# Optimization experiments

Measured on AMD Instinct MI355X. Metric: run time of the kernel, lower is better.

## Reference

```python
import jax, jax.numpy as jnp
import numpy as np

EPS = 1e-6


def setup_inputs() -> dict:
    key = jax.random.key(0)
    kx, ky = jax.random.split(key)
    B, C, H, W = 8, 128, 48, 64
    x = jax.random.normal(kx, (B, C, H, W), dtype=jnp.float32)
    y = jax.random.normal(ky, (B, C, H, W), dtype=jnp.float32)
    return {"x": x, "y": y}


def reference(x, y):
    # x, y: (b, c, h, w)
    b, c, h, w = x.shape
    # torch: x.transpose(2,3).view(b,c,h*w) -> x flattened w-major,
    #        so output channel k = v*h + u corresponds to x[:, :, u, v].
    # corr5[b, v, u, i, j] = sum_c x[b,c,u,v] * y[b,c,i,j]
    corr = jnp.einsum('bcuv,bcij->bvuij', x, y)
    corr = corr.reshape(b, w * h, h, w)  # channel k = v*h + u
    # normalization: ReLU then L2-normalize over the h*w channel dim
    corr = jax.nn.relu(corr)
    norm = jnp.sqrt(jnp.sum(corr * corr, axis=1, keepdims=True) + EPS)
    return corr / norm
```

## Files before the change

kernel.cpp:

```cpp
#include <hip/hip_runtime.h>
#include <hip/hip_bf16.h>

#define NB 8
#define NC 128
#define NH 48
#define NW 64
#define NS 3072
#define EPSF 1e-6f

#define GLOBAL_AS __attribute__((address_space(1)))
#define LDS_AS __attribute__((address_space(3)))

typedef __bf16 bf16x8 __attribute__((ext_vector_type(8)));
typedef float f32x4 __attribute__((ext_vector_type(4)));

__global__ __launch_bounds__(256) void transpose_both(
    const float* __restrict__ x, const float* __restrict__ y,
    __hip_bfloat16* __restrict__ AT, __hip_bfloat16* __restrict__ BT) {
  __shared__ float tile[32][65];
  const int id = blockIdx.x;
  const int b = id & 7;
  const int which = (id >> 3) & 1;
  const int rr = id >> 4;
  const int f0 = (rr % 96) * 32, c0 = (rr / 96) * 64;
  const float* src = which ? y : x;
  __hip_bfloat16* dst = which ? BT : AT;
  const int t = threadIdx.x;

  const int fi = t & 31, ci0 = t >> 5;
  const float* sp = src + ((size_t)b * NC + c0) * NS + f0;
#pragma unroll
  for (int i = 0; i < 8; ++i) {
    int ci = ci0 + i * 8;
    tile[fi][ci] = sp[(size_t)ci * NS + fi];
  }
  __syncthreads();

  const int co = t & 63, fo0 = t >> 6;
#pragma unroll
  for (int i = 0; i < 8; ++i) {
    int fo = fo0 + i * 4;
    int f = f0 + fo;
    int k = which ? f : ((f & 63) * NH + (f >> 6));
    dst[((size_t)b * NS + k) * NC + c0 + co] = __float2bfloat16(tile[fo][co]);
  }
}

template <bool WRITE>
__global__ __launch_bounds__(256, 2) void corr_gemm(
    const __hip_bfloat16* __restrict__ AT,
    const __hip_bfloat16* __restrict__ BT,
    const float* __restrict__ part_in, float* __restrict__ part_out,
    float* __restrict__ out) {
  __shared__ char smem[66560];
  float* rnc = (float*)(smem + 65536);
  const int id = blockIdx.x;
  const int b = id & 7;
  const int tl = id >> 3;
  const int mt = tl / 24, nt = tl - mt * 24;
  const int t = threadIdx.x;
  const int lane = t & 63, wid = t >> 6;
  const int wm = wid >> 1, wn = wid & 1;
  const int l15 = lane & 15, kg = lane >> 4;

  const char* Ag = (const char*)(AT + ((size_t)b * NS + mt * 128) * NC);
  const char* Bg = (const char*)(BT + ((size_t)b * NS + nt * 128) * NC);
  {
    const int lr = lane >> 4, lg = lane & 15;
#pragma unroll
    for (int i = 0; i < 8; ++i) {
      int c = wid * 8 + i;
      int row = c * 4 + lr;
      int g = lg ^ (row & 7);
      int go = row * 256 + g * 16;
      __builtin_amdgcn_global_load_lds((const GLOBAL_AS unsigned*)(Ag + go),
                                       (LDS_AS unsigned*)(smem + c * 1024),
                                       16, 0, 0);
      __builtin_amdgcn_global_load_lds(
          (const GLOBAL_AS unsigned*)(Bg + go),
          (LDS_AS unsigned*)(smem + 32768 + c * 1024), 16, 0, 0);
    }
  }
  if (WRITE) {
    if (t < 128) {
      float s = 0.f;
#pragma unroll
      for (int q = 0; q < 24; ++q)
        s += part_in[(size_t)q * (NB * NS) + (size_t)b * NS + nt * 128 + t];
      rnc[t] = rsqrtf(s + EPSF);
    }
  }
  __syncthreads();

  f32x4 acc[4][4] = {};
  const int rx = l15 & 7;
#pragma unroll
  for (int kk = 0; kk < 4; ++kk) {
    int g = (kk * 4 + kg) ^ rx;
    bf16x8 a[4], bb[4];
#pragma unroll
    for (int mi = 0; mi < 4; ++mi) {
      int row = wm * 64 + mi * 16 + l15;
      a[mi] = *(const bf16x8*)(smem + row * 256 + g * 16);
    }
#pragma unroll
    for (int ni = 0; ni < 4; ++ni) {
      int row = wn * 64 + ni * 16 + l15;
      bb[ni] = *(const bf16x8*)(smem + 32768 + row * 256 + g * 16);
    }
#pragma unroll
    for (int mi = 0; mi < 4; ++mi)
#pragma unroll
      for (int ni = 0; ni < 4; ++ni)
        acc[mi][ni] = __builtin_amdgcn_mfma_f32_16x16x32_bf16(
            a[mi], bb[ni], acc[mi][ni], 0, 0, 0);
  }

  if (!WRITE) {
    float cs[4] = {0.f, 0.f, 0.f, 0.f};
#pragma unroll
    for (int ni = 0; ni < 4; ++ni)
#pragma unroll
      for (int mi = 0; mi < 4; ++mi)
#pragma unroll
        for (int r = 0; r < 4; ++r) {
          float v = fmaxf(acc[mi][ni][r], 0.f);
          cs[ni] += v * v;
        }
#pragma unroll
    for (int ni = 0; ni < 4; ++ni) {
      cs[ni] += __shfl_xor(cs[ni], 16, 64);
      cs[ni] += __shfl_xor(cs[ni], 32, 64);
    }
    __syncthreads();
    float* csum = (float*)smem;
    if (kg == 0) {
#pragma unroll
      for (int ni = 0; ni < 4; ++ni)
        csum[wm * 128 + wn * 64 + ni * 16 + l15] = cs[ni];
    }
    __syncthreads();
    if (t < 128) {
      float s = csum[t] + csum[128 + t];
      part_out[(size_t)mt * (NB * NS) + (size_t)b * NS + nt * 128 + t] = s;
    }
  } else {
    float rnv[4];
#pragma unroll
    for (int ni = 0; ni < 4; ++ni) rnv[ni] = rnc[wn * 64 + ni * 16 + l15];
    __syncthreads();

    float* tf = (float*)smem;
#pragma unroll
    for (int mi = 0; mi < 4; ++mi)
#pragma unroll
      for (int ni = 0; ni < 4; ++ni)
#pragma unroll
        for (int r = 0; r < 4; ++r) {
          int row = wm * 64 + mi * 16 + kg * 4 + r;
          int col = wn * 64 + ni * 16 + l15;
          tf[row * 129 + col] = fmaxf(acc[mi][ni][r], 0.f) * rnv[ni];
        }
    __syncthreads();

    float* ob = out + (size_t)b * NS * NS + (size_t)(mt * 128) * NS + nt * 128;
    const int rsub = t >> 5, c4 = (t & 31) * 4;
#pragma unroll
    for (int it = 0; it < 16; ++it) {
      int row = it * 8 + rsub;
      f32x4 v = *(const f32x4*)&tf[row * 129 + c4];
      *(f32x4*)&ob[(size_t)row * NS + c4] = v;
    }
  }
}

extern "C" void kernel_launch(void* const* d_in, const int* in_sizes, int n_in,
                              void* d_out, int out_size, void* d_ws,
                              size_t ws_size, hipStream_t stream) {
  const float* x = (const float*)d_in[0];
  const float* y = (const float*)d_in[1];
  float* out = (float*)d_out;
  char* ws = (char*)d_ws;

  const size_t AT_OFF = 0;
  const size_t BT_OFF = 6291456;
  const size_t PART_OFF = 12582912;
  const size_t NEED = 14942208;
  if (ws_size < NEED) return;

  __hip_bfloat16* AT = (__hip_bfloat16*)(ws + AT_OFF);
  __hip_bfloat16* BT = (__hip_bfloat16*)(ws + BT_OFF);
  float* part = (float*)(ws + PART_OFF);

  dim3 tb(256);
  transpose_both<<<dim3(3072), tb, 0, stream>>>(x, y, AT, BT);
  corr_gemm<false><<<dim3(4608), tb, 0, stream>>>(AT, BT, nullptr, part,
                                                  nullptr);
  corr_gemm<true><<<dim3(4608), tb, 0, stream>>>(AT, BT, part, nullptr, out);
}
```

Measured before the change: 112.6 us.

## Split output GEMM into wider 128x256 tile kernel with chunked epilogue and nontemporal stores

Separates the partial-norm pass and the output pass into distinct kernels. The output pass now uses 512-thread blocks covering a 128x256 tile, which halves the block count and reuses each A tile across twice the columns. The epilogue stages the tile through LDS in two 64-row chunks and writes it with nontemporal stores. This targets the write-bound output phase, reducing per-block overhead and cache pollution from the roughly 300MB output, at the cost of higher LDS use per block and extra barriers.

```diff
diff --git a/kernel.cpp b/kernel.cpp
--- a/kernel.cpp
+++ b/kernel.cpp
@@ -46,14 +46,10 @@
   }
 }
 
-template <bool WRITE>
-__global__ __launch_bounds__(256, 2) void corr_gemm(
+__global__ __launch_bounds__(256, 2) void corr_part(
     const __hip_bfloat16* __restrict__ AT,
-    const __hip_bfloat16* __restrict__ BT,
-    const float* __restrict__ part_in, float* __restrict__ part_out,
-    float* __restrict__ out) {
-  __shared__ char smem[66560];
-  float* rnc = (float*)(smem + 65536);
+    const __hip_bfloat16* __restrict__ BT, float* __restrict__ part_out) {
+  __shared__ char smem[65536];
   const int id = blockIdx.x;
   const int b = id & 7;
   const int tl = id >> 3;
@@ -81,15 +77,6 @@
           (LDS_AS unsigned*)(smem + 32768 + c * 1024), 16, 0, 0);
     }
   }
-  if (WRITE) {
-    if (t < 128) {
-      float s = 0.f;
-#pragma unroll
-      for (int q = 0; q < 24; ++q)
-        s += part_in[(size_t)q * (NB * NS) + (size_t)b * NS + nt * 128 + t];
-      rnc[t] = rsqrtf(s + EPSF);
-    }
-  }
   __syncthreads();
 
   f32x4 acc[4][4] = {};
@@ -99,15 +86,12 @@
     int g = (kk * 4 + kg) ^ rx;
     bf16x8 a[4], bb[4];
 #pragma unroll
-    for (int mi = 0; mi < 4; ++mi) {
-      int row = wm * 64 + mi * 16 + l15;
-      a[mi] = *(const bf16x8*)(smem + row * 256 + g * 16);
-    }
-#pragma unroll
-    for (int ni = 0; ni < 4; ++ni) {
-      int row = wn * 64 + ni * 16 + l15;
-      bb[ni] = *(const bf16x8*)(smem + 32768 + row * 256 + g * 16);
-    }
+    for (int mi = 0; mi < 4; ++mi)
+      a[mi] = *(const bf16x8*)(smem + (wm * 64 + mi * 16 + l15) * 256 + g * 16);
+#pragma unroll
+    for (int ni = 0; ni < 4; ++ni)
+      bb[ni] = *(const bf16x8*)(smem + 32768 +
+                                (wn * 64 + ni * 16 + l15) * 256 + g * 16);
 #pragma unroll
     for (int mi = 0; mi < 4; ++mi)
 #pragma unroll
@@ -116,61 +100,133 @@
             a[mi], bb[ni], acc[mi][ni], 0, 0, 0);
   }
 
-  if (!WRITE) {
-    float cs[4] = {0.f, 0.f, 0.f, 0.f};
+  float cs[4] = {0.f, 0.f, 0.f, 0.f};
+#pragma unroll
+  for (int ni = 0; ni < 4; ++ni)
+#pragma unroll
+    for (int mi = 0; mi < 4; ++mi)
+#pragma unroll
+      for (int r = 0; r < 4; ++r) {
+        float v = fmaxf(acc[mi][ni][r], 0.f);
+        cs[ni] += v * v;
+      }
+#pragma unroll
+  for (int ni = 0; ni < 4; ++ni) {
+    cs[ni] += __shfl_xor(cs[ni], 16, 64);
+    cs[ni] += __shfl_xor(cs[ni], 32, 64);
+  }
+  __syncthreads();
+  float* csum = (float*)smem;
+  if (kg == 0) {
 #pragma unroll
     for (int ni = 0; ni < 4; ++ni)
+      csum[wm * 128 + wn * 64 + ni * 16 + l15] = cs[ni];
+  }
+  __syncthreads();
+  if (t < 128) {
+    float s = csum[t] + csum[128 + t];
+    part_out[(size_t)mt * (NB * NS) + (size_t)b * NS + nt * 128 + t] = s;
+  }
+}
+
+__global__ __launch_bounds__(512, 2) void corr_out256(
+    const __hip_bfloat16* __restrict__ AT,
+    const __hip_bfloat16* __restrict__ BT, const float* __restrict__ part_in,
+    float* __restrict__ out) {
+  __shared__ char smem[99328];
+  float* rnc = (float*)(smem + 98304);
+  const int id = blockIdx.x;
+  const int b = id & 7;
+  const int tl = id >> 3;
+  const int mt = tl / 12, nt = tl - mt * 12;
+  const int t = threadIdx.x;
+  const int lane = t & 63, wid = t >> 6;
+  const int wm = wid >> 2, wn = wid & 3;
+  const int l15 = lane & 15, kg = lane >> 4;
+
+  const char* Ag = (const char*)(AT + ((size_t)b * NS + mt * 128) * NC);
+  const char* Bg = (const char*)(BT + ((size_t)b * NS + nt * 256) * NC);
+  {
+    const int lr = lane >> 4, lg = lane & 15;
+#pragma unroll
+    for (int i = 0; i < 4; ++i) {
+      int c = wid * 4 + i;
+      int row = c * 4 + lr;
+      int g = lg ^ (row & 7);
+      __builtin_amdgcn_global_load_lds(
+          (const GLOBAL_AS unsigned*)(Ag + row * 256 + g * 16),
+          (LDS_AS unsigned*)(smem + c * 1024), 16, 0, 0);
+    }
+#pragma unroll
+    for (int i = 0; i < 8; ++i) {
+      int c = wid * 8 + i;
+      int row = c * 4 + lr;
+      int g = lg ^ (row & 7);
+      __builtin_amdgcn_global_load_lds(
+          (const GLOBAL_AS unsigned*)(Bg + row * 256 + g * 16),
+          (LDS_AS unsigned*)(smem + 32768 + c * 1024), 16, 0, 0);
+    }
+  }
+  if (t < 256) {
+    float s = 0.f;
+#pragma unroll
+    for (int q = 0; q < 24; ++q)
+      s += part_in[(size_t)q * (NB * NS) + (size_t)b * NS + nt * 256 + t];
+    rnc[t] = rsqrtf(s + EPSF);
+  }
+  __syncthreads();
+
+  f32x4 acc[4][4] = {};
+  const int rx = l15 & 7;
+#pragma unroll
+  for (int kk = 0; kk < 4; ++kk) {
+    int g = (kk * 4 + kg) ^ rx;
+    bf16x8 a[4], bb[4];
+#pragma unroll
+    for (int mi = 0; mi < 4; ++mi)
+      a[mi] = *(const bf16x8*)(smem + (wm * 64 + mi * 16 + l15) * 256 + g * 16);
+#pragma unroll
+    for (int ni = 0; ni < 4; ++ni)
+      bb[ni] = *(const bf16x8*)(smem + 32768 +
+                                (wn * 64 + ni * 16 + l15) * 256 + g * 16);
+#pragma unroll
+    for (int mi = 0; mi < 4; ++mi)
+#pragma unroll
+      for (int ni = 0; ni < 4; ++ni)
+        acc[mi][ni] = __builtin_amdgcn_mfma_f32_16x16x32_bf16(
+            a[mi], bb[ni], acc[mi][ni], 0, 0, 0);
+  }
+
+  float rnv[4];
+#pragma unroll
+  for (int ni = 0; ni < 4; ++ni) rnv[ni] = rnc[wn * 64 + ni * 16 + l15];
+  __syncthreads();
+
+  float* tf = (float*)smem;
+  float* ob = out + (size_t)b * NS * NS + (size_t)(mt * 128) * NS + nt * 256;
+#pragma unroll
+  for (int ch = 0; ch < 2; ++ch) {
+    if (wm == ch) {
 #pragma unroll
       for (int mi = 0; mi < 4; ++mi)
 #pragma unroll
-        for (int r = 0; r < 4; ++r) {
-          float v = fmaxf(acc[mi][ni][r], 0.f);
-          cs[ni] += v * v;
-        }
-#pragma unroll
-    for (int ni = 0; ni < 4; ++ni) {
-      cs[ni] += __shfl_xor(cs[ni], 16, 64);
-      cs[ni] += __shfl_xor(cs[ni], 32, 64);
+        for (int ni = 0; ni < 4; ++ni)
+#pragma unroll
+          for (int r = 0; r < 4; ++r) {
+            int row = mi * 16 + kg * 4 + r;
+            int col = wn * 64 + ni * 16 + l15;
+            tf[row * 258 + col] = fmaxf(acc[mi][ni][r], 0.f) * rnv[ni];
+          }
     }
     __syncthreads();
-    float* csum = (float*)smem;
-    if (kg == 0) {
-#pragma unroll
-      for (int ni = 0; ni < 4; ++ni)
-        csum[wm * 128 + wn * 64 + ni * 16 + l15] = cs[ni];
+#pragma unroll
+    for (int it = 0; it < 8; ++it) {
+      int rl = wid + it * 8;
+      f32x4 v = *(const f32x4*)&tf[rl * 258 + lane * 4];
+      __builtin_nontemporal_store(
+          v, (f32x4*)&ob[(size_t)(ch * 64 + rl) * NS + lane * 4]);
     }
     __syncthreads();
-    if (t < 128) {
-      float s = csum[t] + csum[128 + t];
-      part_out[(size_t)mt * (NB * NS) + (size_t)b * NS + nt * 128 + t] = s;
-    }
-  } else {
-    float rnv[4];
-#pragma unroll
-    for (int ni = 0; ni < 4; ++ni) rnv[ni] = rnc[wn * 64 + ni * 16 + l15];
-    __syncthreads();
-
-    float* tf = (float*)smem;
-#pragma unroll
-    for (int mi = 0; mi < 4; ++mi)
-#pragma unroll
-      for (int ni = 0; ni < 4; ++ni)
-#pragma unroll
-        for (int r = 0; r < 4; ++r) {
-          int row = wm * 64 + mi * 16 + kg * 4 + r;
-          int col = wn * 64 + ni * 16 + l15;
-          tf[row * 129 + col] = fmaxf(acc[mi][ni][r], 0.f) * rnv[ni];
-        }
-    __syncthreads();
-
-    float* ob = out + (size_t)b * NS * NS + (size_t)(mt * 128) * NS + nt * 128;
-    const int rsub = t >> 5, c4 = (t & 31) * 4;
-#pragma unroll
-    for (int it = 0; it < 16; ++it) {
-      int row = it * 8 + rsub;
-      f32x4 v = *(const f32x4*)&tf[row * 129 + c4];
-      *(f32x4*)&ob[(size_t)row * NS + c4] = v;
-    }
   }
 }
 
@@ -192,9 +248,7 @@
   __hip_bfloat16* BT = (__hip_bfloat16*)(ws + BT_OFF);
   float* part = (float*)(ws + PART_OFF);
 
-  dim3 tb(256);
-  transpose_both<<<dim3(3072), tb, 0, stream>>>(x, y, AT, BT);
-  corr_gemm<false><<<dim3(4608), tb, 0, stream>>>(AT, BT, nullptr, part,
-                                                  nullptr);
-  corr_gemm<true><<<dim3(4608), tb, 0, stream>>>(AT, BT, part, nullptr, out);
-}
+  transpose_both<<<dim3(3072), dim3(256), 0, stream>>>(x, y, AT, BT);
+  corr_part<<<dim3(4608), dim3(256), 0, stream>>>(AT, BT, part);
+  corr_out256<<<dim3(2304), dim3(512), 0, stream>>>(AT, BT, part, out);
+}
```

After: 101.6 us. -9.8%, faster.
